# Optimization experiments

Measured on AMD Instinct MI355X. Metric: run time of the kernel, lower is better.

Reference implementation:

```python
import jax, jax.numpy as jnp
import numpy as np

B, NV, NT = 4, 4096, 1024
VDIM, TDIM, HEADS = 1024, 1024, 8

def setup_inputs() -> dict:
    key = jax.random.key(0)
    k1, k2, k3 = jax.random.split(key, 3)
    visual = jax.random.normal(k1, (B, NV, VDIM), dtype=jnp.float32)
    textual = jax.random.normal(k2, (B, NT, TDIM), dtype=jnp.float32)
    # torch Linear(visual_dim, textual_dim, bias=False): y = x @ W.T, W [TDIM, VDIM]
    W = jax.random.normal(k3, (TDIM, VDIM), dtype=jnp.float32) * (1.0 / np.sqrt(VDIM))
    return {"visual": visual, "textual": textual, "W": W}

def reference(visual, textual, W):
    h = HEADS
    visual_context = jnp.einsum('bnv,tv->bnt', visual, W)  # [B, NV, TDIM]
    d = TDIM // h
    q = textual.reshape(B, NT, h, d).transpose(0, 2, 1, 3)         # b h i d
    k = visual_context.reshape(B, NV, h, d).transpose(0, 2, 1, 3)  # b h j d
    sim = jnp.einsum('bhid,bhjd->bhij', q, k)  # no scale, per original
    attn = jax.nn.softmax(sim, axis=-1)
    out = jnp.einsum('bhij,bhjd->bhid', attn, k)  # V = K
    out = out.transpose(0, 2, 1, 3).reshape(B, NT, TDIM)
    return (out, attn)
```

## Files before the change

### kernel.cpp

```cpp
#include <hip/hip_runtime.h>
#include <hip/hip_bf16.h>
#include <math.h>

#define BB    4
#define NV    4096
#define NT    1024
#define VDIM  1024
#define TDIM  1024
#define HEADS 8
#define DHEAD 128
#define KVBLK 64
#define NTILES (NV / KVBLK)

typedef __bf16 bf16x8 __attribute__((ext_vector_type(8)));
typedef float  f32x4  __attribute__((ext_vector_type(4)));

__device__ __forceinline__ bf16x8 load8(const __bf16* p) {
    return *reinterpret_cast<const bf16x8*>(p);
}
__device__ __forceinline__ void store8(__bf16* p, bf16x8 v) {
    *reinterpret_cast<bf16x8*>(p) = v;
}
__device__ __forceinline__ void async16(const __bf16* g, __bf16* l) {
    __builtin_amdgcn_global_load_lds(
        (const __attribute__((address_space(1))) unsigned int*)g,
        (__attribute__((address_space(3))) unsigned int*)l, 16, 0, 0);
}
__device__ __forceinline__ void split8(const float* __restrict__ p,
                                       bf16x8& hi, bf16x8& lo) {
    const f32x4 v0 = *reinterpret_cast<const f32x4*>(p);
    const f32x4 v1 = *reinterpret_cast<const f32x4*>(p + 4);
#pragma unroll
    for (int j = 0; j < 4; j++) {
        const __bf16 h0 = (__bf16)v0[j];
        hi[j] = h0; lo[j] = (__bf16)(v0[j] - (float)h0);
        const __bf16 h1 = (__bf16)v1[j];
        hi[4 + j] = h1; lo[4 + j] = (__bf16)(v1[j] - (float)h1);
    }
}

__global__ __launch_bounds__(256) void gemm1_kernel(
    const float* __restrict__ visual,
    const float* __restrict__ W,
    __bf16* __restrict__ vc_hi,
    __bf16* __restrict__ vc_lo)
{
    const int lane = threadIdx.x & 63;
    const int wave = threadIdx.x >> 6;
    const int wm = wave >> 1, wn = wave & 1;
    const int m0 = blockIdx.y * 128 + wm * 64;
    const int n0 = blockIdx.x * 128 + wn * 64;
    const int lrow = lane & 15;
    const int lk8  = (lane >> 4) * 8;

    f32x4 acc[4][4];
#pragma unroll
    for (int i = 0; i < 4; i++)
#pragma unroll
        for (int j = 0; j < 4; j++) acc[i][j] = (f32x4){0.f, 0.f, 0.f, 0.f};

    for (int k0 = 0; k0 < VDIM; k0 += 32) {
        bf16x8 bh[4], bl[4];
#pragma unroll
        for (int nt = 0; nt < 4; nt++)
            split8(W + (size_t)(n0 + nt * 16 + lrow) * VDIM + k0 + lk8, bh[nt], bl[nt]);
#pragma unroll
        for (int mt = 0; mt < 4; mt++) {
            bf16x8 ah, al;
            split8(visual + (size_t)(m0 + mt * 16 + lrow) * VDIM + k0 + lk8, ah, al);
#pragma unroll
            for (int nt = 0; nt < 4; nt++) {
                acc[mt][nt] = __builtin_amdgcn_mfma_f32_16x16x32_bf16(ah, bh[nt], acc[mt][nt], 0, 0, 0);
                acc[mt][nt] = __builtin_amdgcn_mfma_f32_16x16x32_bf16(ah, bl[nt], acc[mt][nt], 0, 0, 0);
                acc[mt][nt] = __builtin_amdgcn_mfma_f32_16x16x32_bf16(al, bh[nt], acc[mt][nt], 0, 0, 0);
            }
        }
    }

    const int r0 = (lane >> 4) * 4;
#pragma unroll
    for (int mt = 0; mt < 4; mt++)
#pragma unroll
        for (int nt = 0; nt < 4; nt++)
#pragma unroll
            for (int r = 0; r < 4; r++) {
                const int row = m0 + mt * 16 + r0 + r;
                const int col = n0 + nt * 16 + lrow;
                const float v = acc[mt][nt][r];
                const __bf16 h = (__bf16)v;
                const __bf16 lo = (__bf16)(v - (float)h);
                const size_t idx = (size_t)row * TDIM + col;
                vc_hi[idx] = h;
                vc_lo[idx] = lo;
            }
}

__global__ __launch_bounds__(256) void transpose_kernel(
    const __bf16* __restrict__ vc_hi,
    __bf16* __restrict__ kT)
{
    __shared__ __bf16 tile[64][72];
    const int bh = blockIdx.z;
    const int b = bh >> 3, h = bh & 7;
    const int kv0 = blockIdx.x * 64;
    const int d0  = blockIdx.y * 64;
    const int t = threadIdx.x;

#pragma unroll
    for (int it = 0; it < 2; it++) {
        const int kvl = (t >> 3) + it * 32;
        const int dl  = (t & 7) * 8;
        bf16x8 v = load8(vc_hi + (size_t)(b * NV + kv0 + kvl) * TDIM + h * DHEAD + d0 + dl);
#pragma unroll
        for (int j = 0; j < 8; j++) tile[kvl][dl + j] = v[j];
    }
    __syncthreads();
#pragma unroll
    for (int it = 0; it < 2; it++) {
        const int dl  = (t >> 3) + it * 32;
        const int kvl = (t & 7) * 8;
        bf16x8 v;
#pragma unroll
        for (int j = 0; j < 8; j++) v[j] = tile[kvl + j][dl];
        store8(kT + (size_t)(bh * DHEAD + d0 + dl) * NV + kv0 + kvl, v);
    }
}

__global__ __launch_bounds__(256, 2) void attn_kernel(
    const float* __restrict__ textual,
    const __bf16* __restrict__ vc_hi,
    const __bf16* __restrict__ vc_lo,
    const __bf16* __restrict__ kT,
    float* __restrict__ out,
    float* __restrict__ attn)
{
    __shared__ __bf16 kbuf[2][2][KVBLK][128];
    __shared__ __bf16 lds_p[4][16][72];

    const int bh = blockIdx.y;
    const int b = bh >> 3, h = bh & 7;
    const int q0 = blockIdx.x * 64;
    const int lane = threadIdx.x & 63;
    const int wave = threadIdx.x >> 6;
    const int lrow = lane & 15;
    const int quad = lane >> 4;
    const int lk8  = quad * 8;
    const int qw = q0 + wave * 16;
    const int sw = lrow & 7;

    bf16x8 qh[4], ql[4];
#pragma unroll
    for (int ks = 0; ks < 4; ks++)
        split8(textual + (size_t)(b * NT + qw + lrow) * TDIM + h * DHEAD + ks * 32 + lk8,
               qh[ks], ql[ks]);

    const __bf16* khi_base = vc_hi + (size_t)b * NV * TDIM + h * DHEAD;
    const __bf16* klo_base = vc_lo + (size_t)b * NV * TDIM + h * DHEAD;

    const int tid = (int)threadIdx.x;
    auto stage = [&](int kt, int d) {
        const int kv0s = kt * KVBLK;
#pragma unroll
        for (int i = 0; i < 4; i++) {
            const int cidx = i * 256 + tid;
            const int kv = cidx >> 4;
            const int ch = (cidx & 15) ^ (kv & 7);
            const size_t goff = (size_t)(kv0s + kv) * TDIM + ch * 8;
            const int lbase = (i * 256 + (tid & ~63)) * 8;
            async16(khi_base + goff, &kbuf[d][0][0][0] + lbase);
            async16(klo_base + goff, &kbuf[d][1][0][0] + lbase);
        }
    };

    float m_run[4], l_run[4];
#pragma unroll
    for (int r = 0; r < 4; r++) { m_run[r] = -INFINITY; l_run[r] = 0.f; }

    stage(0, 0);
    __syncthreads();
    for (int kt = 0; kt < NTILES; kt++) {
        const int cur = kt & 1;
        if (kt + 1 < NTILES) stage(kt + 1, cur ^ 1);
        f32x4 acc[4];
#pragma unroll
        for (int c = 0; c < 4; c++) acc[c] = (f32x4){0.f, 0.f, 0.f, 0.f};
#pragma unroll
        for (int c = 0; c < 4; c++) {
#pragma unroll
            for (int ks = 0; ks < 4; ks++) {
                const int sc = ((ks * 4 + quad) ^ sw) * 8;
                bf16x8 kh = load8(&kbuf[cur][0][c * 16 + lrow][sc]);
                bf16x8 kl = load8(&kbuf[cur][1][c * 16 + lrow][sc]);
                acc[c] = __builtin_amdgcn_mfma_f32_16x16x32_bf16(qh[ks], kh, acc[c], 0, 0, 0);
                acc[c] = __builtin_amdgcn_mfma_f32_16x16x32_bf16(qh[ks], kl, acc[c], 0, 0, 0);
                acc[c] = __builtin_amdgcn_mfma_f32_16x16x32_bf16(ql[ks], kh, acc[c], 0, 0, 0);
            }
        }
#pragma unroll
        for (int r = 0; r < 4; r++) {
            float tm = fmaxf(fmaxf(acc[0][r], acc[1][r]), fmaxf(acc[2][r], acc[3][r]));
#pragma unroll
            for (int off = 1; off < 16; off <<= 1)
                tm = fmaxf(tm, __shfl_xor(tm, off, 64));
            const float nm = fmaxf(m_run[r], tm);
            float ps = __expf(acc[0][r] - nm) + __expf(acc[1][r] - nm) +
                       __expf(acc[2][r] - nm) + __expf(acc[3][r] - nm);
#pragma unroll
            for (int off = 1; off < 16; off <<= 1)
                ps += __shfl_xor(ps, off, 64);
            l_run[r] = l_run[r] * __expf(m_run[r] - nm) + ps;
            m_run[r] = nm;
        }
        __syncthreads();
    }

    float inv_l[4];
#pragma unroll
    for (int r = 0; r < 4; r++) inv_l[r] = 1.0f / l_run[r];

    f32x4 oacc[8];
#pragma unroll
    for (int c = 0; c < 8; c++) oacc[c] = (f32x4){0.f, 0.f, 0.f, 0.f};

    float* attn_base = attn + (size_t)bh * NT * NV;
    const __bf16* kT_base = kT + (size_t)bh * DHEAD * NV;

    stage(0, 0);
    __syncthreads();
    for (int kt = 0; kt < NTILES; kt++) {
        const int cur = kt & 1;
        const int kv0 = kt * KVBLK;
        if (kt + 1 < NTILES) stage(kt + 1, cur ^ 1);
        f32x4 acc[4];
#pragma unroll
        for (int c = 0; c < 4; c++) acc[c] = (f32x4){0.f, 0.f, 0.f, 0.f};
#pragma unroll
        for (int c = 0; c < 4; c++) {
#pragma unroll
            for (int ks = 0; ks < 4; ks++) {
                const int sc = ((ks * 4 + quad) ^ sw) * 8;
                bf16x8 kh = load8(&kbuf[cur][0][c * 16 + lrow][sc]);
                bf16x8 kl = load8(&kbuf[cur][1][c * 16 + lrow][sc]);
                acc[c] = __builtin_amdgcn_mfma_f32_16x16x32_bf16(qh[ks], kh, acc[c], 0, 0, 0);
                acc[c] = __builtin_amdgcn_mfma_f32_16x16x32_bf16(qh[ks], kl, acc[c], 0, 0, 0);
                acc[c] = __builtin_amdgcn_mfma_f32_16x16x32_bf16(ql[ks], kh, acc[c], 0, 0, 0);
            }
        }
#pragma unroll
        for (int c = 0; c < 4; c++)
#pragma unroll
            for (int r = 0; r < 4; r++) {
                const float p = __expf(acc[c][r] - m_run[r]) * inv_l[r];
                lds_p[wave][quad * 4 + r][c * 16 + lrow] = (__bf16)p;
                attn_base[(size_t)(qw + quad * 4 + r) * NV + kv0 + c * 16 + lrow] = p;
            }

#pragma unroll
        for (int kss = 0; kss < 2; kss++) {
            bf16x8 ap = load8(&lds_p[wave][lrow][kss * 32 + lk8]);
#pragma unroll
            for (int ct = 0; ct < 8; ct++) {
                bf16x8 bk = load8(kT_base + (size_t)(ct * 16 + lrow) * NV + kv0 + kss * 32 + lk8);
                oacc[ct] = __builtin_amdgcn_mfma_f32_16x16x32_bf16(ap, bk, oacc[ct], 0, 0, 0);
            }
        }
        __syncthreads();
    }

#pragma unroll
    for (int ct = 0; ct < 8; ct++)
#pragma unroll
        for (int r = 0; r < 4; r++) {
            const int qrow = qw + quad * 4 + r;
            const int dcol = ct * 16 + lrow;
            out[(size_t)(b * NT + qrow) * TDIM + h * DHEAD + dcol] = oacc[ct][r];
        }
}

extern "C" void kernel_launch(void* const* d_in, const int* in_sizes, int n_in,
                              void* d_out, int out_size, void* d_ws, size_t ws_size,
                              hipStream_t stream)
{
    const float* visual  = (const float*)d_in[0];
    const float* textual = (const float*)d_in[1];
    const float* W       = (const float*)d_in[2];

    float* out  = (float*)d_out;
    float* attn = out + (size_t)BB * NT * TDIM;

    const size_t VC_ELEMS = (size_t)BB * NV * TDIM;
    __bf16* vc_hi = (__bf16*)d_ws;
    __bf16* vc_lo = vc_hi + VC_ELEMS;
    __bf16* kT    = vc_lo + VC_ELEMS;

    gemm1_kernel<<<dim3(TDIM / 128, (BB * NV) / 128), 256, 0, stream>>>(
        visual, W, vc_hi, vc_lo);
    transpose_kernel<<<dim3(NV / 64, DHEAD / 64, BB * HEADS), 256, 0, stream>>>(
        vc_hi, kT);
    attn_kernel<<<dim3(NT / 64, BB * HEADS), 256, 0, stream>>>(
        textual, vc_hi, vc_lo, kT, out, attn);
}
```

Before: 1.272 ms.

## Stage gemm1 operand tiles through double-buffered LDS with async global loads

The projection GEMM now copies 128x32 fp32 tiles of visual and W into double-buffered shared memory using async global-to-LDS loads with an XOR swizzle. Each wave then reads its fragments from LDS instead of issuing strided global loads per wave. Loading the next k-slice while the current one is computed is meant to hide global memory latency and to cut redundant global traffic across waves. In exchange it adds a barrier per k step, uses 64KB of LDS per block, and adds a launch-bounds occupancy hint.

```diff
diff --git a/kernel.cpp b/kernel.cpp
--- a/kernel.cpp
+++ b/kernel.cpp
@@ -21,7 +21,7 @@
 __device__ __forceinline__ void store8(__bf16* p, bf16x8 v) {
     *reinterpret_cast<bf16x8*>(p) = v;
 }
-__device__ __forceinline__ void async16(const __bf16* g, __bf16* l) {
+__device__ __forceinline__ void async16(const void* g, void* l) {
     __builtin_amdgcn_global_load_lds(
         (const __attribute__((address_space(1))) unsigned int*)g,
         (__attribute__((address_space(3))) unsigned int*)l, 16, 0, 0);
@@ -38,20 +38,34 @@
         hi[4 + j] = h1; lo[4 + j] = (__bf16)(v1[j] - (float)h1);
     }
 }
-
-__global__ __launch_bounds__(256) void gemm1_kernel(
+__device__ __forceinline__ void split44(const f32x4 v0, const f32x4 v1,
+                                        bf16x8& hi, bf16x8& lo) {
+#pragma unroll
+    for (int j = 0; j < 4; j++) {
+        const __bf16 h0 = (__bf16)v0[j];
+        hi[j] = h0; lo[j] = (__bf16)(v0[j] - (float)h0);
+        const __bf16 h1 = (__bf16)v1[j];
+        hi[4 + j] = h1; lo[4 + j] = (__bf16)(v1[j] - (float)h1);
+    }
+}
+
+__global__ __launch_bounds__(256, 2) void gemm1_kernel(
     const float* __restrict__ visual,
     const float* __restrict__ W,
     __bf16* __restrict__ vc_hi,
     __bf16* __restrict__ vc_lo)
 {
+    __shared__ float Abuf[2][128][32];
+    __shared__ float Bbuf[2][128][32];
+
     const int lane = threadIdx.x & 63;
     const int wave = threadIdx.x >> 6;
     const int wm = wave >> 1, wn = wave & 1;
-    const int m0 = blockIdx.y * 128 + wm * 64;
-    const int n0 = blockIdx.x * 128 + wn * 64;
+    const int bm0 = blockIdx.y * 128;
+    const int bn0 = blockIdx.x * 128;
     const int lrow = lane & 15;
-    const int lk8  = (lane >> 4) * 8;
+    const int quad = lane >> 4;
+    const int tid = (int)threadIdx.x;
 
     f32x4 acc[4][4];
 #pragma unroll
@@ -59,15 +73,46 @@
 #pragma unroll
         for (int j = 0; j < 4; j++) acc[i][j] = (f32x4){0.f, 0.f, 0.f, 0.f};
 
-    for (int k0 = 0; k0 < VDIM; k0 += 32) {
+    auto stage = [&](int k0, int d) {
+#pragma unroll
+        for (int i = 0; i < 4; i++) {
+            const int cidx = i * 256 + tid;
+            const int row = cidx >> 3;
+            const int sc  = (cidx & 7) ^ (row & 7);
+            const int lbase = (i * 256 + (tid & ~63)) * 4;
+            async16(visual + (size_t)(bm0 + row) * VDIM + k0 + sc * 4,
+                    &Abuf[d][0][0] + lbase);
+            async16(W + (size_t)(bn0 + row) * VDIM + k0 + sc * 4,
+                    &Bbuf[d][0][0] + lbase);
+        }
+    };
+
+    stage(0, 0);
+    __syncthreads();
+
+    for (int ks = 0; ks < VDIM / 32; ks++) {
+        const int cur = ks & 1;
+        if (ks + 1 < VDIM / 32) stage((ks + 1) * 32, cur ^ 1);
+
         bf16x8 bh[4], bl[4];
 #pragma unroll
-        for (int nt = 0; nt < 4; nt++)
-            split8(W + (size_t)(n0 + nt * 16 + lrow) * VDIM + k0 + lk8, bh[nt], bl[nt]);
+        for (int nt = 0; nt < 4; nt++) {
+            const int row = wn * 64 + nt * 16 + lrow;
+            const int c0 = (quad * 2) ^ (row & 7);
+            const int c1 = (quad * 2 + 1) ^ (row & 7);
+            const f32x4 v0 = *reinterpret_cast<const f32x4*>(&Bbuf[cur][row][c0 * 4]);
+            const f32x4 v1 = *reinterpret_cast<const f32x4*>(&Bbuf[cur][row][c1 * 4]);
+            split44(v0, v1, bh[nt], bl[nt]);
+        }
 #pragma unroll
         for (int mt = 0; mt < 4; mt++) {
+            const int row = wm * 64 + mt * 16 + lrow;
+            const int c0 = (quad * 2) ^ (row & 7);
+            const int c1 = (quad * 2 + 1) ^ (row & 7);
+            const f32x4 v0 = *reinterpret_cast<const f32x4*>(&Abuf[cur][row][c0 * 4]);
+            const f32x4 v1 = *reinterpret_cast<const f32x4*>(&Abuf[cur][row][c1 * 4]);
             bf16x8 ah, al;
-            split8(visual + (size_t)(m0 + mt * 16 + lrow) * VDIM + k0 + lk8, ah, al);
+            split44(v0, v1, ah, al);
 #pragma unroll
             for (int nt = 0; nt < 4; nt++) {
                 acc[mt][nt] = __builtin_amdgcn_mfma_f32_16x16x32_bf16(ah, bh[nt], acc[mt][nt], 0, 0, 0);
@@ -75,9 +120,12 @@
                 acc[mt][nt] = __builtin_amdgcn_mfma_f32_16x16x32_bf16(al, bh[nt], acc[mt][nt], 0, 0, 0);
             }
         }
-    }
-
-    const int r0 = (lane >> 4) * 4;
+        __syncthreads();
+    }
+
+    const int m0 = bm0 + wm * 64;
+    const int n0 = bn0 + wn * 64;
+    const int r0 = quad * 4;
 #pragma unroll
     for (int mt = 0; mt < 4; mt++)
 #pragma unroll
```

Result: faster. 1.164 ms (-8.5%).
